# Kernel tuning notes

Measured on AMD Instinct MI355X. Metric: run time of the kernel, lower is better.

The kernel has to match this reference:

```python
import jax, jax.numpy as jnp
import numpy as np

U = I = 4096; E = 128; K = 4; D = E // K; R = 3; B = 512; L = 100
LAMB = 0.5; L2NORM = 1e-4; EPS = 1e-8


def _l2norm(x, axis):
    n = jnp.sqrt(jnp.sum(x * x, axis=axis, keepdims=True))
    return x / jnp.maximum(n, 1e-12)


def setup_inputs() -> dict:
    key = jax.random.key(0)
    ks = jax.random.split(key, 16)
    def adj(k, shape, p=0.01):
        return jax.random.bernoulli(k, p, shape).astype(jnp.float32)
    relation_mats = adj(ks[0], (R, U, I))
    item_graphs = adj(ks[1], (R, I, I))
    train_matrix = relation_mats[0]
    inp = {
        "user": jax.random.randint(ks[2], (B, 1), 0, U),
        "item": jax.random.randint(ks[3], (B, L), 0, I),
        "user_embedding": jax.random.normal(ks[4], (U, E), jnp.float32) * 0.1,
        "item_embedding": jax.random.normal(ks[5], (I, E), jnp.float32) * 0.1,
        "mgnn_weight": jax.random.normal(ks[6], (R,), jnp.float32),
        "item_behaviour_W": jax.random.normal(ks[7], (R, E, E), jnp.float32) * 0.05,
        "item_propagate_W": jax.random.normal(ks[8], (R, E, E), jnp.float32) * 0.05,
        "W": jax.random.normal(ks[9], (E, E), jnp.float32) * 0.05,
        "W_K": jax.random.normal(ks[10], (K, D, E), jnp.float32) * 0.05,
        "B_K": jax.random.normal(ks[11], (K, D), jnp.float32) * 0.05,
        "train_matrix": train_matrix,
        "relation_mats": relation_mats,
        "item_graphs": item_graphs,
        "item_graph_degree": item_graphs.sum(axis=2, keepdims=True),  # [R,I,1]
        "user_behaviour_degree": relation_mats.sum(axis=2).T,  # [U,R]
    }
    return inp


def reference(user, item, user_embedding, item_embedding, mgnn_weight,
              item_behaviour_W, item_propagate_W, W, W_K, B_K,
              train_matrix, relation_mats, item_graphs, item_graph_degree,
              user_behaviour_degree):
    # behaviour weighting: [U,R]
    total_weight = user_behaviour_degree @ mgnn_weight[:, None]  # [U,1]
    ubw = user_behaviour_degree * mgnn_weight[None, :] / (total_weight + EPS)

    # K-head projections (relation-independent; original recomputes identically per relation)
    s_i = _l2norm(jax.nn.relu(jnp.einsum('kde,ie->kdi', W_K, item_embedding) + B_K[..., None]), axis=1)  # [K,D,I]
    s_u0 = _l2norm(jax.nn.relu(jnp.einsum('kde,ue->kdu', W_K, user_embedding) + B_K[..., None]), axis=1)  # [K,D,U]
    s_u0 = jnp.transpose(s_u0, (2, 0, 1))  # [U,K,D]

    ue_blocks = user_embedding.reshape(U, K, D)
    logits = jnp.einsum('ukd,kdi->kui', ue_blocks, s_i)  # [K,U,I]
    r = jax.nn.softmax(logits, axis=0)  # exp / sum over K heads

    user_feature = jnp.zeros((U, E), user_embedding.dtype)
    score2 = jnp.zeros((B, L), user_embedding.dtype)
    for i in range(R):
        rel = relation_mats[i]  # [U,I]
        # item-item propagation
        tip = ((item_graphs[i] @ item_embedding) / (item_graph_degree[i] + EPS)) @ item_propagate_W[i]  # [I,E]
        tmp_item_emb = tip[item]  # [B,L,E]
        # attention-weighted user-item propagation per head
        s_u = s_u0 + jnp.einsum('kui,kdi->ukd', r * rel[None], s_i)  # [U,K,D]
        tun = _l2norm(s_u, axis=2).reshape(U, E)  # tmp_user_neighbour
        tuinp = (rel @ tip) / (user_behaviour_degree[:, i:i + 1] + EPS)  # [U,E]
        user_feature = user_feature + ubw[:, i:i + 1] * tun
        proj = tuinp @ item_behaviour_W[i]  # [U,E]
        score2 = score2 + jnp.sum(proj[user[:, 0]][:, None, :] * tmp_item_emb, axis=2)
    score2 = score2 / R

    item_feature = (train_matrix.T @ user_embedding) @ W  # [I,E]
    user_feature = user_feature @ W  # [U,E]

    uf = user_feature[user[:, 0]][:, None, :]  # [B,1,E]
    itf = item_feature[item]  # [B,L,E]
    score1 = jnp.sum(uf * itf, axis=2)  # [B,L]
    scores = score1 + LAMB * score2
    L2_loss = L2NORM * (L * jnp.sum(uf ** 2) + jnp.sum(itf ** 2))
    return scores, L2_loss
```

## Files before the change

### kernel.cpp

```cpp
#include <hip/hip_runtime.h>

#define NU 4096
#define NI 4096
#define NR 3
#define NB 512
#define NL 100
#define FEPS 1e-8f

#define WS_SI    0
#define WS_EMBW  524288
#define WS_TIP   2097152
#define WS_UEW   3670016
#define WS_ITEMF 4194304
#define WS_WTUN  4718592
#define WS_PROJ  4915200
#define WS_UF    5111808
#define WS_UF2P  5177344
#define WS_ITF2P 5177856
#define WS_BMT   5190656

__global__ void k_prep(const float* __restrict__ iemb, const float* __restrict__ ipW,
                       const float* __restrict__ uemb, const float* __restrict__ Wm,
                       const float* __restrict__ WK, const float* __restrict__ BK,
                       const float* __restrict__ tm,
                       float* __restrict__ embW, float* __restrict__ uew,
                       float* __restrict__ si, unsigned long long* __restrict__ bmT) {
  int t = threadIdx.x;
  int bid = blockIdx.x;
  if (bid < 4096) {
    __shared__ unsigned char nib[4][256];
    const float4* r4 = (const float4*)(tm + (size_t)bid * NI);
#pragma unroll
    for (int q = 0; q < 4; ++q) {
      float4 v = r4[q * 256 + t];
      unsigned m = 0;
      if (v.x != 0.f) m |= 1u;
      if (v.y != 0.f) m |= 2u;
      if (v.z != 0.f) m |= 4u;
      if (v.w != 0.f) m |= 8u;
      nib[q][t] = (unsigned char)m;
    }
    __syncthreads();
    if (t < 64) {
      unsigned long long mm = 0;
#pragma unroll
      for (int j = 0; j < 16; ++j) {
        int e = t * 16 + j;
        mm |= (unsigned long long)nib[e >> 8][e & 255] << (4 * j);
      }
      bmT[(size_t)t * NU + bid] = mm;
    }
  } else if (bid < 5120) {
    __shared__ __align__(16) float shbuf[2048];
    int lb = bid - 4096;
    int batch = lb >> 8, rb = lb & 255;
    const float* in;
    const float* Wp;
    float* outp;
    if (batch < 3) {
      in = iemb;
      Wp = ipW + (size_t)batch * 16384;
      outp = embW + (size_t)batch * NI * 128;
    } else {
      in = uemb; Wp = Wm; outp = uew;
    }
    const float4* in4 = (const float4*)(in + (size_t)rb * 2048);
    for (int c = t; c < 512; c += 256) ((float4*)shbuf)[c] = in4[c];
    __syncthreads();
    int c = t & 127, g = t >> 7;
    float acc[8];
#pragma unroll
    for (int rr = 0; rr < 8; ++rr) acc[rr] = 0.f;
    for (int e = 0; e < 128; ++e) {
      float wv = Wp[e * 128 + c];
#pragma unroll
      for (int rr = 0; rr < 8; ++rr) acc[rr] += shbuf[(g * 8 + rr) * 128 + e] * wv;
    }
#pragma unroll
    for (int rr = 0; rr < 8; ++rr) outp[((size_t)rb * 16 + g * 8 + rr) * 128 + c] = acc[rr];
  } else {
    __shared__ __align__(16) float embs2[256];
    int tl = t & 127, half = t >> 7;
    int item = (bid - 5120) * 2 + half;
    float* embs = embs2 + half * 128;
    if (tl < 32) ((float4*)embs)[tl] = ((const float4*)(iemb + (size_t)item * 128))[tl];
    __syncthreads();
    float acc = BK[tl];
    const float4* wk4 = (const float4*)(WK + (size_t)tl * 128);
    const float4* e4 = (const float4*)embs;
#pragma unroll 8
    for (int cc = 0; cc < 32; ++cc) {
      float4 w = wk4[cc], v = e4[cc];
      acc += w.x * v.x + w.y * v.y + w.z * v.z + w.w * v.w;
    }
    acc = fmaxf(acc, 0.f);
    float sq = acc * acc;
#pragma unroll
    for (int m = 1; m <= 16; m <<= 1) sq += __shfl_xor(sq, m);
    si[(size_t)item * 128 + tl] = acc / fmaxf(sqrtf(sq), 1e-12f);
  }
}

__global__ void k_scan(const float* __restrict__ G, const float* __restrict__ deg,
                       const float* __restrict__ embW, float* __restrict__ tip) {
  int gid = blockIdx.x;
  int t = threadIdx.x;
  int r = gid >> 12;
  const float4* row4 = (const float4*)(G + (size_t)gid * NI);
  __shared__ int nz[512];
  __shared__ int cnt;
  __shared__ float4 red[8][32];
  if (t == 0) cnt = 0;
  __syncthreads();
#pragma unroll
  for (int c = 0; c < 4; ++c) {
    int idx4 = c * 256 + t;
    float4 v = row4[idx4];
    int j0 = idx4 << 2;
    if (v.x != 0.f) nz[atomicAdd(&cnt, 1)] = j0;
    if (v.y != 0.f) nz[atomicAdd(&cnt, 1)] = j0 + 1;
    if (v.z != 0.f) nz[atomicAdd(&cnt, 1)] = j0 + 2;
    if (v.w != 0.f) nz[atomicAdd(&cnt, 1)] = j0 + 3;
  }
  __syncthreads();
  int n = min(cnt, 512);
  int g = t >> 5, f = t & 31;
  float4 acc = {0.f, 0.f, 0.f, 0.f};
  const float4* e4 = (const float4*)(embW + (size_t)r * NI * 128);
  for (int p = g; p < n; p += 8) {
    float4 v = e4[(size_t)nz[p] * 32 + f];
    acc.x += v.x; acc.y += v.y; acc.z += v.z; acc.w += v.w;
  }
  red[g][f] = acc;
  __syncthreads();
  if (t < 32) {
    float4 s = red[0][t];
#pragma unroll
    for (int q = 1; q < 8; ++q) {
      float4 v = red[q][t];
      s.x += v.x; s.y += v.y; s.z += v.z; s.w += v.w;
    }
    float inv = 1.f / (deg[gid] + FEPS);
    s.x *= inv; s.y *= inv; s.z *= inv; s.w *= inv;
    ((float4*)(tip + (size_t)gid * 128))[t] = s;
  }
}

__global__ void k_mid(const unsigned long long* __restrict__ bmT,
                      const float* __restrict__ uew, float* __restrict__ itemf,
                      const int* __restrict__ user, const float* __restrict__ relm,
                      const float* __restrict__ si, const float* __restrict__ tip,
                      const float* __restrict__ uemb, const float* __restrict__ WK,
                      const float* __restrict__ BK, const float* __restrict__ ibW,
                      const float* __restrict__ ubd, const float* __restrict__ mw,
                      float* __restrict__ wtun, float* __restrict__ proj) {
  int t = threadIdx.x;
  int bid = blockIdx.x;
  if (bid < 4096) {
    int i = bid;
    int ct = i >> 6;
    unsigned long long bitm = 1ull << (i & 63);
    __shared__ int lst[192];
    __shared__ int cnt2;
    __shared__ float red2[3][128];
    if (t == 0) cnt2 = 0;
    __syncthreads();
    const unsigned long long* col = bmT + (size_t)ct * NU;
#pragma unroll
    for (int cc = 0; cc < 16; ++cc) {
      unsigned long long m = col[cc * 256 + t];
      if (m & bitm) lst[atomicAdd(&cnt2, 1)] = cc * 256 + t;
    }
    __syncthreads();
    int n = min(cnt2, 192);
    int w = t >> 6, l = t & 63;
    float ax = 0.f, ay = 0.f;
    const float2* uew2 = (const float2*)uew;
    for (int p = w; p < n; p += 4) {
      float2 v = uew2[(size_t)lst[p] * 64 + l];
      ax += v.x; ay += v.y;
    }
    if (w > 0) { red2[w - 1][2 * l] = ax; red2[w - 1][2 * l + 1] = ay; }
    __syncthreads();
    if (w == 0) {
      float2 o;
      o.x = ax + red2[0][2 * l] + red2[1][2 * l] + red2[2][2 * l];
      o.y = ay + red2[0][2 * l + 1] + red2[1][2 * l + 1] + red2[2][2 * l + 1];
      ((float2*)(itemf + (size_t)i * 128))[l] = o;
    }
  } else {
    int ub = bid - 4096;
    int r = ub >> 9, b = ub & 511;
    int u = user[b];
    const float* rel = relm + ((size_t)r * NU + u) * NI;
    __shared__ int nz[512];
    __shared__ int cnt;
    __shared__ __align__(16) float uel[128];
    __shared__ float redA[4][128];
    __shared__ float redB[4][128];
    __shared__ float tu[128];
    if (t == 0) cnt = 0;
    if (t < 32) ((float4*)uel)[t] = ((const float4*)(uemb + (size_t)u * 128))[t];
    __syncthreads();
    const float4* rel4 = (const float4*)rel;
#pragma unroll
    for (int c = 0; c < 4; ++c) {
      int idx4 = c * 256 + t;
      float4 v = rel4[idx4];
      int j0 = idx4 << 2;
      if (v.x != 0.f) nz[atomicAdd(&cnt, 1)] = j0;
      if (v.y != 0.f) nz[atomicAdd(&cnt, 1)] = j0 + 1;
      if (v.z != 0.f) nz[atomicAdd(&cnt, 1)] = j0 + 2;
      if (v.w != 0.f) nz[atomicAdd(&cnt, 1)] = j0 + 3;
    }
    __syncthreads();
    int n = min(cnt, 512);
    int wid = t >> 6, lane = t & 63;
    int k = lane >> 4;
    float2 myue = ((const float2*)uel)[lane];
    float sux = 0.f, suy = 0.f, tpx = 0.f, tpy = 0.f;
    const float2* si2 = (const float2*)si;
    const float2* tip2 = (const float2*)(tip + (size_t)r * NI * 128);
    for (int p = wid; p < n; p += 4) {
      int i = nz[p];
      float2 sv = si2[(size_t)i * 64 + lane];
      float lg = myue.x * sv.x + myue.y * sv.y;
      lg += __shfl_xor(lg, 1);
      lg += __shfl_xor(lg, 2);
      lg += __shfl_xor(lg, 4);
      lg += __shfl_xor(lg, 8);
      float l0 = __shfl(lg, 0), l1 = __shfl(lg, 16), l2 = __shfl(lg, 32), l3 = __shfl(lg, 48);
      float mx = fmaxf(fmaxf(l0, l1), fmaxf(l2, l3));
      float e0 = __expf(l0 - mx), e1 = __expf(l1 - mx), e2 = __expf(l2 - mx), e3 = __expf(l3 - mx);
      float inv = 1.f / (e0 + e1 + e2 + e3);
      float myr = (k == 0 ? e0 : k == 1 ? e1 : k == 2 ? e2 : e3) * inv;
      sux += myr * sv.x;
      suy += myr * sv.y;
      float2 tv = tip2[(size_t)i * 64 + lane];
      tpx += tv.x;
      tpy += tv.y;
    }
    redA[wid][2 * lane] = sux; redA[wid][2 * lane + 1] = suy;
    redB[wid][2 * lane] = tpx; redB[wid][2 * lane + 1] = tpy;
    __syncthreads();
    if (t < 128) {
      float suv = redA[0][t] + redA[1][t] + redA[2][t] + redA[3][t];
      float tipv = redB[0][t] + redB[1][t] + redB[2][t] + redB[3][t];
      float a = BK[t];
      const float4* wk4 = (const float4*)(WK + (size_t)t * 128);
      const float4* ue4 = (const float4*)uel;
#pragma unroll 8
      for (int c = 0; c < 32; ++c) {
        float4 w = wk4[c], v = ue4[c];
        a += w.x * v.x + w.y * v.y + w.z * v.z + w.w * v.w;
      }
      a = fmaxf(a, 0.f);
      float sq = a * a;
#pragma unroll
      for (int m = 1; m <= 16; m <<= 1) sq += __shfl_xor(sq, m);
      float su = a / fmaxf(sqrtf(sq), 1e-12f) + suv;
      float sq2 = su * su;
#pragma unroll
      for (int m = 1; m <= 16; m <<= 1) sq2 += __shfl_xor(sq2, m);
      float tun = su / fmaxf(sqrtf(sq2), 1e-12f);
      float d0 = ubd[u * 3], d1 = ubd[u * 3 + 1], d2 = ubd[u * 3 + 2];
      float w0 = mw[0], w1 = mw[1], w2 = mw[2];
      float tw = d0 * w0 + d1 * w1 + d2 * w2;
      float dr = (r == 0 ? d0 : r == 1 ? d1 : d2);
      float wr = (r == 0 ? w0 : r == 1 ? w1 : w2);
      wtun[(size_t)(b * 3 + r) * 128 + t] = (dr * wr / (tw + FEPS)) * tun;
      tu[t] = tipv / (dr + FEPS);
    }
    __syncthreads();
    int ep = t & 127, hh = t >> 7;
    const float* Wb = ibW + (size_t)r * 16384;
    float pacc = 0.f;
    for (int e = hh * 64; e < hh * 64 + 64; ++e) pacc += tu[e] * Wb[e * 128 + ep];
    redA[hh][ep] = pacc;
    __syncthreads();
    if (hh == 0) proj[(size_t)(b * 3 + r) * 128 + ep] = redA[0][ep] + redA[1][ep];
  }
}

__global__ void k_uf(const float* __restrict__ wtun, const float* __restrict__ Wm,
                     float* __restrict__ uf, float* __restrict__ uf2p) {
  int b = blockIdx.x, t = threadIdx.x;
  __shared__ float comb[128];
  __shared__ float part[2];
  comb[t] = wtun[(size_t)(b * 3) * 128 + t] + wtun[(size_t)(b * 3 + 1) * 128 + t] +
            wtun[(size_t)(b * 3 + 2) * 128 + t];
  __syncthreads();
  float acc = 0.f;
  for (int e = 0; e < 128; ++e) acc += comb[e] * Wm[e * 128 + t];
  uf[(size_t)b * 128 + t] = acc;
  float sq = acc * acc;
#pragma unroll
  for (int m = 1; m <= 32; m <<= 1) sq += __shfl_xor(sq, m);
  if ((t & 63) == 0) part[t >> 6] = sq;
  __syncthreads();
  if (t == 0) uf2p[b] = part[0] + part[1];
}

__global__ void k_score(const int* __restrict__ item, const float* __restrict__ itemf,
                        const float* __restrict__ uf, const float* __restrict__ tip,
                        const float* __restrict__ proj, float* __restrict__ out,
                        float* __restrict__ itf2p) {
  int t = threadIdx.x, wid = t >> 6, lane = t & 63;
  int idx = blockIdx.x * 4 + wid;
  int b = idx / NL;
  int it = item[idx];
  float2 av = ((const float2*)(itemf + (size_t)it * 128))[lane];
  float2 cv = ((const float2*)(uf + (size_t)b * 128))[lane];
  float s1 = av.x * cv.x + av.y * cv.y;
  float sqi = av.x * av.x + av.y * av.y;
  float s2 = 0.f;
#pragma unroll
  for (int r = 0; r < 3; ++r) {
    float2 tv = ((const float2*)(tip + ((size_t)r * NI + it) * 128))[lane];
    float2 pv = ((const float2*)(proj + (size_t)(b * 3 + r) * 128))[lane];
    s2 += tv.x * pv.x + tv.y * pv.y;
  }
#pragma unroll
  for (int m = 1; m <= 32; m <<= 1) {
    s1 += __shfl_xor(s1, m);
    s2 += __shfl_xor(s2, m);
    sqi += __shfl_xor(sqi, m);
  }
  if (lane == 0) out[idx] = s1 + 0.5f * (s2 * (1.f / 3.f));
  __shared__ float sh[4];
  if (lane == 0) sh[wid] = sqi;
  __syncthreads();
  if (t == 0) itf2p[blockIdx.x] = sh[0] + sh[1] + sh[2] + sh[3];
}

__global__ void k_final(const float* __restrict__ itf2p, const float* __restrict__ uf2p,
                        float* __restrict__ out) {
  int t = threadIdx.x;
  float v = 0.f;
  for (int i = t; i < 12800; i += 256) v += itf2p[i];
  float vu = 0.f;
  for (int i = t; i < NB; i += 256) vu += uf2p[i];
  v += 100.f * vu;
#pragma unroll
  for (int m = 1; m <= 32; m <<= 1) v += __shfl_xor(v, m);
  __shared__ float sh[4];
  if ((t & 63) == 0) sh[t >> 6] = v;
  __syncthreads();
  if (t == 0) out[NB * NL] = 1e-4f * (sh[0] + sh[1] + sh[2] + sh[3]);
}

extern "C" void kernel_launch(void* const* d_in, const int* in_sizes, int n_in,
                              void* d_out, int out_size, void* d_ws, size_t ws_size,
                              hipStream_t stream) {
  (void)in_sizes; (void)n_in; (void)out_size; (void)ws_size;
  const int* user = (const int*)d_in[0];
  const int* item = (const int*)d_in[1];
  const float* uemb = (const float*)d_in[2];
  const float* iemb = (const float*)d_in[3];
  const float* mw = (const float*)d_in[4];
  const float* ibW = (const float*)d_in[5];
  const float* ipW = (const float*)d_in[6];
  const float* Wm = (const float*)d_in[7];
  const float* WK = (const float*)d_in[8];
  const float* BK = (const float*)d_in[9];
  const float* tm = (const float*)d_in[10];
  const float* relm = (const float*)d_in[11];
  const float* ig = (const float*)d_in[12];
  const float* igd = (const float*)d_in[13];
  const float* ubd = (const float*)d_in[14];
  float* out = (float*)d_out;
  float* ws = (float*)d_ws;
  unsigned long long* bmT = (unsigned long long*)(ws + WS_BMT);

  k_prep<<<7168, 256, 0, stream>>>(iemb, ipW, uemb, Wm, WK, BK, tm,
                                   ws + WS_EMBW, ws + WS_UEW, ws + WS_SI, bmT);
  k_scan<<<NR * NI, 256, 0, stream>>>(ig, igd, ws + WS_EMBW, ws + WS_TIP);
  k_mid<<<5632, 256, 0, stream>>>(bmT, ws + WS_UEW, ws + WS_ITEMF, user, relm,
                                  ws + WS_SI, ws + WS_TIP, uemb, WK, BK, ibW,
                                  ubd, mw, ws + WS_WTUN, ws + WS_PROJ);
  k_uf<<<NB, 128, 0, stream>>>(ws + WS_WTUN, Wm, ws + WS_UF, ws + WS_UF2P);
  k_score<<<12800, 256, 0, stream>>>(item, ws + WS_ITEMF, ws + WS_UF, ws + WS_TIP,
                                     ws + WS_PROJ, out, ws + WS_ITF2P);
  k_final<<<1, 256, 0, stream>>>(ws + WS_ITF2P, ws + WS_UF2P, out);
}
```

Before: 191.4 us.

## Aggregate raw item embeddings before applying propagate weights, merge scan into prep

The code now uses associativity: (G·E)·Wp = G·(E·Wp). The sparse item-graph aggregation therefore gathers raw item embeddings instead of per-relation pre-multiplied ones, and the 128x128 propagate-weight GEMM runs on the aggregated rows afterwards. The graph scan moves into the first kernel so it runs alongside the bitmask, user-embedding and K-head work. This removes one serial launch dependency and gives all three relations a shared gather source. The old middle kernel is split into an item/tip transform kernel and a user kernel, which adds a launch but keeps the total kernel count the same.

```diff
diff --git a/kernel.cpp b/kernel.cpp
--- a/kernel.cpp
+++ b/kernel.cpp
@@ -7,23 +7,23 @@
 #define NL 100
 #define FEPS 1e-8f
 
-#define WS_SI    0
-#define WS_EMBW  524288
-#define WS_TIP   2097152
-#define WS_UEW   3670016
-#define WS_ITEMF 4194304
-#define WS_WTUN  4718592
-#define WS_PROJ  4915200
-#define WS_UF    5111808
-#define WS_UF2P  5177344
-#define WS_ITF2P 5177856
-#define WS_BMT   5190656
-
-__global__ void k_prep(const float* __restrict__ iemb, const float* __restrict__ ipW,
-                       const float* __restrict__ uemb, const float* __restrict__ Wm,
-                       const float* __restrict__ WK, const float* __restrict__ BK,
-                       const float* __restrict__ tm,
-                       float* __restrict__ embW, float* __restrict__ uew,
+#define WS_SI     0
+#define WS_AGGRAW 524288
+#define WS_TIP    2097152
+#define WS_UEW    3670016
+#define WS_ITEMF  4194304
+#define WS_WTUN   4718592
+#define WS_PROJ   4915200
+#define WS_UF     5111808
+#define WS_UF2P   5177344
+#define WS_ITF2P  5177856
+#define WS_BMT    5190656
+
+__global__ void k_mega(const float* __restrict__ iemb, const float* __restrict__ uemb,
+                       const float* __restrict__ Wm, const float* __restrict__ WK,
+                       const float* __restrict__ BK, const float* __restrict__ tm,
+                       const float* __restrict__ G, const float* __restrict__ deg,
+                       float* __restrict__ aggraw, float* __restrict__ uew,
                        float* __restrict__ si, unsigned long long* __restrict__ bmT) {
   int t = threadIdx.x;
   int bid = blockIdx.x;
@@ -50,21 +50,50 @@
       }
       bmT[(size_t)t * NU + bid] = mm;
     }
-  } else if (bid < 5120) {
+  } else if (bid < 16384) {
+    int gid = bid - 4096;
+    const float4* row4 = (const float4*)(G + (size_t)gid * NI);
+    __shared__ int nz[512];
+    __shared__ int cnt;
+    __shared__ float4 red[8][32];
+    if (t == 0) cnt = 0;
+    __syncthreads();
+#pragma unroll
+    for (int c = 0; c < 4; ++c) {
+      int idx4 = c * 256 + t;
+      float4 v = row4[idx4];
+      int j0 = idx4 << 2;
+      if (v.x != 0.f) nz[atomicAdd(&cnt, 1)] = j0;
+      if (v.y != 0.f) nz[atomicAdd(&cnt, 1)] = j0 + 1;
+      if (v.z != 0.f) nz[atomicAdd(&cnt, 1)] = j0 + 2;
+      if (v.w != 0.f) nz[atomicAdd(&cnt, 1)] = j0 + 3;
+    }
+    __syncthreads();
+    int n = min(cnt, 512);
+    int g = t >> 5, f = t & 31;
+    float4 acc = {0.f, 0.f, 0.f, 0.f};
+    const float4* e4 = (const float4*)iemb;
+    for (int p = g; p < n; p += 8) {
+      float4 v = e4[(size_t)nz[p] * 32 + f];
+      acc.x += v.x; acc.y += v.y; acc.z += v.z; acc.w += v.w;
+    }
+    red[g][f] = acc;
+    __syncthreads();
+    if (t < 32) {
+      float4 s = red[0][t];
+#pragma unroll
+      for (int q = 1; q < 8; ++q) {
+        float4 v = red[q][t];
+        s.x += v.x; s.y += v.y; s.z += v.z; s.w += v.w;
+      }
+      float inv = 1.f / (deg[gid] + FEPS);
+      s.x *= inv; s.y *= inv; s.z *= inv; s.w *= inv;
+      ((float4*)(aggraw + (size_t)gid * 128))[t] = s;
+    }
+  } else if (bid < 16640) {
     __shared__ __align__(16) float shbuf[2048];
-    int lb = bid - 4096;
-    int batch = lb >> 8, rb = lb & 255;
-    const float* in;
-    const float* Wp;
-    float* outp;
-    if (batch < 3) {
-      in = iemb;
-      Wp = ipW + (size_t)batch * 16384;
-      outp = embW + (size_t)batch * NI * 128;
-    } else {
-      in = uemb; Wp = Wm; outp = uew;
-    }
-    const float4* in4 = (const float4*)(in + (size_t)rb * 2048);
+    int rb = bid - 16384;
+    const float4* in4 = (const float4*)(uemb + (size_t)rb * 2048);
     for (int c = t; c < 512; c += 256) ((float4*)shbuf)[c] = in4[c];
     __syncthreads();
     int c = t & 127, g = t >> 7;
@@ -72,16 +101,16 @@
 #pragma unroll
     for (int rr = 0; rr < 8; ++rr) acc[rr] = 0.f;
     for (int e = 0; e < 128; ++e) {
-      float wv = Wp[e * 128 + c];
+      float wv = Wm[e * 128 + c];
 #pragma unroll
       for (int rr = 0; rr < 8; ++rr) acc[rr] += shbuf[(g * 8 + rr) * 128 + e] * wv;
     }
 #pragma unroll
-    for (int rr = 0; rr < 8; ++rr) outp[((size_t)rb * 16 + g * 8 + rr) * 128 + c] = acc[rr];
+    for (int rr = 0; rr < 8; ++rr) uew[((size_t)rb * 16 + g * 8 + rr) * 128 + c] = acc[rr];
   } else {
     __shared__ __align__(16) float embs2[256];
     int tl = t & 127, half = t >> 7;
-    int item = (bid - 5120) * 2 + half;
+    int item = (bid - 16640) * 2 + half;
     float* embs = embs2 + half * 128;
     if (tl < 32) ((float4*)embs)[tl] = ((const float4*)(iemb + (size_t)item * 128))[tl];
     __syncthreads();
@@ -101,63 +130,33 @@
   }
 }
 
-__global__ void k_scan(const float* __restrict__ G, const float* __restrict__ deg,
-                       const float* __restrict__ embW, float* __restrict__ tip) {
-  int gid = blockIdx.x;
-  int t = threadIdx.x;
-  int r = gid >> 12;
-  const float4* row4 = (const float4*)(G + (size_t)gid * NI);
-  __shared__ int nz[512];
-  __shared__ int cnt;
-  __shared__ float4 red[8][32];
-  if (t == 0) cnt = 0;
-  __syncthreads();
-#pragma unroll
-  for (int c = 0; c < 4; ++c) {
-    int idx4 = c * 256 + t;
-    float4 v = row4[idx4];
-    int j0 = idx4 << 2;
-    if (v.x != 0.f) nz[atomicAdd(&cnt, 1)] = j0;
-    if (v.y != 0.f) nz[atomicAdd(&cnt, 1)] = j0 + 1;
-    if (v.z != 0.f) nz[atomicAdd(&cnt, 1)] = j0 + 2;
-    if (v.w != 0.f) nz[atomicAdd(&cnt, 1)] = j0 + 3;
-  }
-  __syncthreads();
-  int n = min(cnt, 512);
-  int g = t >> 5, f = t & 31;
-  float4 acc = {0.f, 0.f, 0.f, 0.f};
-  const float4* e4 = (const float4*)(embW + (size_t)r * NI * 128);
-  for (int p = g; p < n; p += 8) {
-    float4 v = e4[(size_t)nz[p] * 32 + f];
-    acc.x += v.x; acc.y += v.y; acc.z += v.z; acc.w += v.w;
-  }
-  red[g][f] = acc;
-  __syncthreads();
-  if (t < 32) {
-    float4 s = red[0][t];
-#pragma unroll
-    for (int q = 1; q < 8; ++q) {
-      float4 v = red[q][t];
-      s.x += v.x; s.y += v.y; s.z += v.z; s.w += v.w;
-    }
-    float inv = 1.f / (deg[gid] + FEPS);
-    s.x *= inv; s.y *= inv; s.z *= inv; s.w *= inv;
-    ((float4*)(tip + (size_t)gid * 128))[t] = s;
-  }
-}
-
-__global__ void k_mid(const unsigned long long* __restrict__ bmT,
-                      const float* __restrict__ uew, float* __restrict__ itemf,
-                      const int* __restrict__ user, const float* __restrict__ relm,
-                      const float* __restrict__ si, const float* __restrict__ tip,
-                      const float* __restrict__ uemb, const float* __restrict__ WK,
-                      const float* __restrict__ BK, const float* __restrict__ ibW,
-                      const float* __restrict__ ubd, const float* __restrict__ mw,
-                      float* __restrict__ wtun, float* __restrict__ proj) {
+__global__ void k_mid2(const float* __restrict__ aggraw, const float* __restrict__ ipW,
+                       const unsigned long long* __restrict__ bmT,
+                       const float* __restrict__ uew,
+                       float* __restrict__ tip, float* __restrict__ itemf) {
   int t = threadIdx.x;
   int bid = blockIdx.x;
-  if (bid < 4096) {
-    int i = bid;
+  if (bid < 768) {
+    __shared__ __align__(16) float shbuf[2048];
+    int rb = bid;
+    int batch = rb >> 8;
+    const float* Wp = ipW + (size_t)batch * 16384;
+    const float4* in4 = (const float4*)(aggraw + (size_t)rb * 2048);
+    for (int c = t; c < 512; c += 256) ((float4*)shbuf)[c] = in4[c];
+    __syncthreads();
+    int c = t & 127, g = t >> 7;
+    float acc[8];
+#pragma unroll
+    for (int rr = 0; rr < 8; ++rr) acc[rr] = 0.f;
+    for (int e = 0; e < 128; ++e) {
+      float wv = Wp[e * 128 + c];
+#pragma unroll
+      for (int rr = 0; rr < 8; ++rr) acc[rr] += shbuf[(g * 8 + rr) * 128 + e] * wv;
+    }
+#pragma unroll
+    for (int rr = 0; rr < 8; ++rr) tip[((size_t)rb * 16 + g * 8 + rr) * 128 + c] = acc[rr];
+  } else {
+    int i = bid - 768;
     int ct = i >> 6;
     unsigned long long bitm = 1ull << (i & 63);
     __shared__ int lst[192];
@@ -188,98 +187,106 @@
       o.y = ay + red2[0][2 * l + 1] + red2[1][2 * l + 1] + red2[2][2 * l + 1];
       ((float2*)(itemf + (size_t)i * 128))[l] = o;
     }
-  } else {
-    int ub = bid - 4096;
-    int r = ub >> 9, b = ub & 511;
-    int u = user[b];
-    const float* rel = relm + ((size_t)r * NU + u) * NI;
-    __shared__ int nz[512];
-    __shared__ int cnt;
-    __shared__ __align__(16) float uel[128];
-    __shared__ float redA[4][128];
-    __shared__ float redB[4][128];
-    __shared__ float tu[128];
-    if (t == 0) cnt = 0;
-    if (t < 32) ((float4*)uel)[t] = ((const float4*)(uemb + (size_t)u * 128))[t];
-    __syncthreads();
-    const float4* rel4 = (const float4*)rel;
-#pragma unroll
-    for (int c = 0; c < 4; ++c) {
-      int idx4 = c * 256 + t;
-      float4 v = rel4[idx4];
-      int j0 = idx4 << 2;
-      if (v.x != 0.f) nz[atomicAdd(&cnt, 1)] = j0;
-      if (v.y != 0.f) nz[atomicAdd(&cnt, 1)] = j0 + 1;
-      if (v.z != 0.f) nz[atomicAdd(&cnt, 1)] = j0 + 2;
-      if (v.w != 0.f) nz[atomicAdd(&cnt, 1)] = j0 + 3;
-    }
-    __syncthreads();
-    int n = min(cnt, 512);
-    int wid = t >> 6, lane = t & 63;
-    int k = lane >> 4;
-    float2 myue = ((const float2*)uel)[lane];
-    float sux = 0.f, suy = 0.f, tpx = 0.f, tpy = 0.f;
-    const float2* si2 = (const float2*)si;
-    const float2* tip2 = (const float2*)(tip + (size_t)r * NI * 128);
-    for (int p = wid; p < n; p += 4) {
-      int i = nz[p];
-      float2 sv = si2[(size_t)i * 64 + lane];
-      float lg = myue.x * sv.x + myue.y * sv.y;
-      lg += __shfl_xor(lg, 1);
-      lg += __shfl_xor(lg, 2);
-      lg += __shfl_xor(lg, 4);
-      lg += __shfl_xor(lg, 8);
-      float l0 = __shfl(lg, 0), l1 = __shfl(lg, 16), l2 = __shfl(lg, 32), l3 = __shfl(lg, 48);
-      float mx = fmaxf(fmaxf(l0, l1), fmaxf(l2, l3));
-      float e0 = __expf(l0 - mx), e1 = __expf(l1 - mx), e2 = __expf(l2 - mx), e3 = __expf(l3 - mx);
-      float inv = 1.f / (e0 + e1 + e2 + e3);
-      float myr = (k == 0 ? e0 : k == 1 ? e1 : k == 2 ? e2 : e3) * inv;
-      sux += myr * sv.x;
-      suy += myr * sv.y;
-      float2 tv = tip2[(size_t)i * 64 + lane];
-      tpx += tv.x;
-      tpy += tv.y;
-    }
-    redA[wid][2 * lane] = sux; redA[wid][2 * lane + 1] = suy;
-    redB[wid][2 * lane] = tpx; redB[wid][2 * lane + 1] = tpy;
-    __syncthreads();
-    if (t < 128) {
-      float suv = redA[0][t] + redA[1][t] + redA[2][t] + redA[3][t];
-      float tipv = redB[0][t] + redB[1][t] + redB[2][t] + redB[3][t];
-      float a = BK[t];
-      const float4* wk4 = (const float4*)(WK + (size_t)t * 128);
-      const float4* ue4 = (const float4*)uel;
+  }
+}
+
+__global__ void k_user(const int* __restrict__ user, const float* __restrict__ relm,
+                       const float* __restrict__ si, const float* __restrict__ tip,
+                       const float* __restrict__ uemb, const float* __restrict__ WK,
+                       const float* __restrict__ BK, const float* __restrict__ ibW,
+                       const float* __restrict__ ubd, const float* __restrict__ mw,
+                       float* __restrict__ wtun, float* __restrict__ proj) {
+  int ub = blockIdx.x;
+  int r = ub >> 9, b = ub & 511;
+  int t = threadIdx.x;
+  int u = user[b];
+  const float* rel = relm + ((size_t)r * NU + u) * NI;
+  __shared__ int nz[512];
+  __shared__ int cnt;
+  __shared__ __align__(16) float uel[128];
+  __shared__ float redA[4][128];
+  __shared__ float redB[4][128];
+  __shared__ float tu[128];
+  if (t == 0) cnt = 0;
+  if (t < 32) ((float4*)uel)[t] = ((const float4*)(uemb + (size_t)u * 128))[t];
+  __syncthreads();
+  const float4* rel4 = (const float4*)rel;
+#pragma unroll
+  for (int c = 0; c < 4; ++c) {
+    int idx4 = c * 256 + t;
+    float4 v = rel4[idx4];
+    int j0 = idx4 << 2;
+    if (v.x != 0.f) nz[atomicAdd(&cnt, 1)] = j0;
+    if (v.y != 0.f) nz[atomicAdd(&cnt, 1)] = j0 + 1;
+    if (v.z != 0.f) nz[atomicAdd(&cnt, 1)] = j0 + 2;
+    if (v.w != 0.f) nz[atomicAdd(&cnt, 1)] = j0 + 3;
+  }
+  __syncthreads();
+  int n = min(cnt, 512);
+  int wid = t >> 6, lane = t & 63;
+  int k = lane >> 4;
+  float2 myue = ((const float2*)uel)[lane];
+  float sux = 0.f, suy = 0.f, tpx = 0.f, tpy = 0.f;
+  const float2* si2 = (const float2*)si;
+  const float2* tip2 = (const float2*)(tip + (size_t)r * NI * 128);
+  for (int p = wid; p < n; p += 4) {
+    int i = nz[p];
+    float2 sv = si2[(size_t)i * 64 + lane];
+    float lg = myue.x * sv.x + myue.y * sv.y;
+    lg += __shfl_xor(lg, 1);
+    lg += __shfl_xor(lg, 2);
+    lg += __shfl_xor(lg, 4);
+    lg += __shfl_xor(lg, 8);
+    float l0 = __shfl(lg, 0), l1 = __shfl(lg, 16), l2 = __shfl(lg, 32), l3 = __shfl(lg, 48);
+    float mx = fmaxf(fmaxf(l0, l1), fmaxf(l2, l3));
+    float e0 = __expf(l0 - mx), e1 = __expf(l1 - mx), e2 = __expf(l2 - mx), e3 = __expf(l3 - mx);
+    float inv = 1.f / (e0 + e1 + e2 + e3);
+    float myr = (k == 0 ? e0 : k == 1 ? e1 : k == 2 ? e2 : e3) * inv;
+    sux += myr * sv.x;
+    suy += myr * sv.y;
+    float2 tv = tip2[(size_t)i * 64 + lane];
+    tpx += tv.x;
+    tpy += tv.y;
+  }
+  redA[wid][2 * lane] = sux; redA[wid][2 * lane + 1] = suy;
+  redB[wid][2 * lane] = tpx; redB[wid][2 * lane + 1] = tpy;
+  __syncthreads();
+  if (t < 128) {
+    float suv = redA[0][t] + redA[1][t] + redA[2][t] + redA[3][t];
+    float tipv = redB[0][t] + redB[1][t] + redB[2][t] + redB[3][t];
+    float a = BK[t];
+    const float4* wk4 = (const float4*)(WK + (size_t)t * 128);
+    const float4* ue4 = (const float4*)uel;
 #pragma unroll 8
-      for (int c = 0; c < 32; ++c) {
-        float4 w = wk4[c], v = ue4[c];
-        a += w.x * v.x + w.y * v.y + w.z * v.z + w.w * v.w;
-      }
-      a = fmaxf(a, 0.f);
-      float sq = a * a;
-#pragma unroll
-      for (int m = 1; m <= 16; m <<= 1) sq += __shfl_xor(sq, m);
-      float su = a / fmaxf(sqrtf(sq), 1e-12f) + suv;
-      float sq2 = su * su;
-#pragma unroll
-      for (int m = 1; m <= 16; m <<= 1) sq2 += __shfl_xor(sq2, m);
-      float tun = su / fmaxf(sqrtf(sq2), 1e-12f);
-      float d0 = ubd[u * 3], d1 = ubd[u * 3 + 1], d2 = ubd[u * 3 + 2];
-      float w0 = mw[0], w1 = mw[1], w2 = mw[2];
-      float tw = d0 * w0 + d1 * w1 + d2 * w2;
-      float dr = (r == 0 ? d0 : r == 1 ? d1 : d2);
-      float wr = (r == 0 ? w0 : r == 1 ? w1 : w2);
-      wtun[(size_t)(b * 3 + r) * 128 + t] = (dr * wr / (tw + FEPS)) * tun;
-      tu[t] = tipv / (dr + FEPS);
-    }
-    __syncthreads();
-    int ep = t & 127, hh = t >> 7;
-    const float* Wb = ibW + (size_t)r * 16384;
-    float pacc = 0.f;
-    for (int e = hh * 64; e < hh * 64 + 64; ++e) pacc += tu[e] * Wb[e * 128 + ep];
-    redA[hh][ep] = pacc;
-    __syncthreads();
-    if (hh == 0) proj[(size_t)(b * 3 + r) * 128 + ep] = redA[0][ep] + redA[1][ep];
-  }
+    for (int c = 0; c < 32; ++c) {
+      float4 w = wk4[c], v = ue4[c];
+      a += w.x * v.x + w.y * v.y + w.z * v.z + w.w * v.w;
+    }
+    a = fmaxf(a, 0.f);
+    float sq = a * a;
+#pragma unroll
+    for (int m = 1; m <= 16; m <<= 1) sq += __shfl_xor(sq, m);
+    float su = a / fmaxf(sqrtf(sq), 1e-12f) + suv;
+    float sq2 = su * su;
+#pragma unroll
+    for (int m = 1; m <= 16; m <<= 1) sq2 += __shfl_xor(sq2, m);
+    float tun = su / fmaxf(sqrtf(sq2), 1e-12f);
+    float d0 = ubd[u * 3], d1 = ubd[u * 3 + 1], d2 = ubd[u * 3 + 2];
+    float w0 = mw[0], w1 = mw[1], w2 = mw[2];
+    float tw = d0 * w0 + d1 * w1 + d2 * w2;
+    float dr = (r == 0 ? d0 : r == 1 ? d1 : d2);
+    float wr = (r == 0 ? w0 : r == 1 ? w1 : w2);
+    wtun[(size_t)(b * 3 + r) * 128 + t] = (dr * wr / (tw + FEPS)) * tun;
+    tu[t] = tipv / (dr + FEPS);
+  }
+  __syncthreads();
+  int ep = t & 127, hh = t >> 7;
+  const float* Wb = ibW + (size_t)r * 16384;
+  float pacc = 0.f;
+  for (int e = hh * 64; e < hh * 64 + 64; ++e) pacc += tu[e] * Wb[e * 128 + ep];
+  redA[hh][ep] = pacc;
+  __syncthreads();
+  if (hh == 0) proj[(size_t)(b * 3 + r) * 128 + ep] = redA[0][ep] + redA[1][ep];
 }
 
 __global__ void k_uf(const float* __restrict__ wtun, const float* __restrict__ Wm,
@@ -372,12 +379,12 @@
   float* ws = (float*)d_ws;
   unsigned long long* bmT = (unsigned long long*)(ws + WS_BMT);
 
-  k_prep<<<7168, 256, 0, stream>>>(iemb, ipW, uemb, Wm, WK, BK, tm,
-                                   ws + WS_EMBW, ws + WS_UEW, ws + WS_SI, bmT);
-  k_scan<<<NR * NI, 256, 0, stream>>>(ig, igd, ws + WS_EMBW, ws + WS_TIP);
-  k_mid<<<5632, 256, 0, stream>>>(bmT, ws + WS_UEW, ws + WS_ITEMF, user, relm,
-                                  ws + WS_SI, ws + WS_TIP, uemb, WK, BK, ibW,
-                                  ubd, mw, ws + WS_WTUN, ws + WS_PROJ);
+  k_mega<<<18688, 256, 0, stream>>>(iemb, uemb, Wm, WK, BK, tm, ig, igd,
+                                    ws + WS_AGGRAW, ws + WS_UEW, ws + WS_SI, bmT);
+  k_mid2<<<4864, 256, 0, stream>>>(ws + WS_AGGRAW, ipW, bmT, ws + WS_UEW,
+                                   ws + WS_TIP, ws + WS_ITEMF);
+  k_user<<<1536, 256, 0, stream>>>(user, relm, ws + WS_SI, ws + WS_TIP, uemb, WK, BK,
+                                   ibW, ubd, mw, ws + WS_WTUN, ws + WS_PROJ);
   k_uf<<<NB, 128, 0, stream>>>(ws + WS_WTUN, Wm, ws + WS_UF, ws + WS_UF2P);
   k_score<<<12800, 256, 0, stream>>>(item, ws + WS_ITEMF, ws + WS_UF, ws + WS_TIP,
                                      ws + WS_PROJ, out, ws + WS_ITF2P);
```

New measurement: 191.9 us. Within noise of the previous version (+0.2%).
